# Kernel optimization log

Measured on AMD Instinct MI355X. Metric: run time of the kernel, lower is better.

Reference implementation:

```python
import jax, jax.numpy as jnp
import numpy as np

B, O, GRID = 2048, 48, 112
SIGMA = 5.0


def setup_inputs() -> dict:
    key = jax.random.key(0)
    k1, k2, k3, k4, k5 = jax.random.split(key, 5)
    s = float(GRID - 1)
    xL = jax.random.uniform(k1, (B,), dtype=jnp.float32) * s
    yL = jax.random.uniform(k2, (B,), dtype=jnp.float32) * s
    obj_list = jax.random.uniform(k3, (B, O, 2), dtype=jnp.float32) * s
    obj_num = jax.random.randint(k4, (B,), 0, O + 1, dtype=jnp.int32)
    road_mask = jax.random.randint(k5, (B, GRID, GRID), 0, 2, dtype=jnp.int32)
    return {"xL": xL, "yL": yL, "obj_list": obj_list, "obj_num": obj_num,
            "road_mask": road_mask, "H": GRID, "W": GRID}


def reference(xL, yL, obj_list, obj_num, road_mask, H, W):
    # Faithful vectorization of batch_gaussian_tensor_obj.
    # exp(-(dx^2+dy^2)/(2s^2)) is separable: exp(-dx^2/..) * exp(-dy^2/..),
    # so per-object splats reduce to a batched matmul over the object axis.
    inv = 1.0 / (2.0 * SIGMA * SIGMA)
    x = jnp.arange(H, dtype=jnp.float32)  # row coordinate grid
    y = jnp.arange(W, dtype=jnp.float32)  # col coordinate grid

    # positive goal gaussian, rank-1 outer product per batch element
    gx = jnp.exp(-((x[None, :] - xL[:, None]) ** 2) * inv)  # [B,H]
    gy = jnp.exp(-((y[None, :] - yL[:, None]) ** 2) * inv)  # [B,W]
    goal = gx[:, :, None] * gy[:, None, :]                   # [B,H,W]

    # negative object gaussians; note original swaps xy: xo=xy[1], yo=xy[0]
    xo = obj_list[:, :, 1]  # [B,O] row coords
    yo = obj_list[:, :, 0]  # [B,O] col coords
    ex = jnp.exp(-((x[None, None, :] - xo[:, :, None]) ** 2) * inv)  # [B,O,H]
    ey = jnp.exp(-((y[None, None, :] - yo[:, :, None]) ** 2) * inv)  # [B,O,W]
    valid = (jnp.arange(O)[None, :] < obj_num[:, None]).astype(jnp.float32)  # [B,O]
    obj = jnp.einsum('boh,bow->bhw', ex * valid[:, :, None], ey)     # [B,H,W]

    channel = 0.5 + 0.5 * goal - 0.5 * obj
    channel = jnp.where(road_mask == 0, 0.0, channel)
    return channel
```

## Files before the change

### kernel.cpp

```cpp
#include <hip/hip_runtime.h>

#define GRID_N 112
#define O_MAX 48
#define HW_N (GRID_N * GRID_N)
#define NT 448
#define LSTR 72

typedef _Float16 half8  __attribute__((ext_vector_type(8)));
typedef _Float16 half2v __attribute__((ext_vector_type(2)));
typedef float    f32x4  __attribute__((ext_vector_type(4)));

__global__ __launch_bounds__(NT) void goalmap_kernel(
    const float* __restrict__ xL, const float* __restrict__ yL,
    const float* __restrict__ obj_list, const int* __restrict__ obj_num,
    const int* __restrict__ road_mask, float* __restrict__ out)
{
    constexpr float INV = 1.0f / (2.0f * 5.0f * 5.0f);

    __shared__ _Float16 eyT[GRID_N * LSTR];

    const int b   = blockIdx.x;
    const int tid = threadIdx.x;
    const int n   = obj_num[b];
    const float xl = xL[b];
    const float yl = yL[b];
    const float* ob = obj_list + (size_t)b * O_MAX * 2;

    const int lane = tid & 63;
    const int wid  = tid >> 6;
    const int m    = lane & 15;
    const int quad = lane >> 4;

    const int* rm = road_mask + (size_t)b * HW_N;
    float*     op = out       + (size_t)b * HW_N;

    const int ksteps = (n >= 32) ? 2 : 1;

    float eyy0[8], eyy1[8];
    #pragma unroll
    for (int it = 0; it < 8; ++it) {
        int i  = tid + it * NT;
        int o0 = (i & 31) * 2;
        eyy0[it] = (o0     < n) ? ob[o0 * 2]     : 0.f;
        eyy1[it] = (o0 + 1 < n) ? ob[o0 * 2 + 2] : 0.f;
    }
    float ax0[8], ax1[8];
    #pragma unroll
    for (int j = 0; j < 8; ++j) {
        int k = quad * 8 + j;
        ax0[j] = (k < n)      ? ob[k * 2 + 1]        : 0.f;
        ax1[j] = (k + 32 < n) ? ob[(k + 32) * 2 + 1] : 0.f;
    }

    int mpf[7][4];
    const int base_h = wid * 16 + quad * 4;
    #pragma unroll
    for (int twp = 0; twp < 3; ++twp) {
        int base = base_h * GRID_N + twp * 16 + m;
        #pragma unroll
        for (int r = 0; r < 4; ++r)
            mpf[twp][r] = rm[base + r * GRID_N];
    }

    #pragma unroll
    for (int it = 0; it < 8; ++it) {
        int i   = tid + it * NT;
        int pos = i >> 5;
        int o0  = (i & 31) * 2;
        float fp = (float)pos;
        half2v v;
        {
            float val = 0.f;
            if (o0 <= n) {
                float cy = (o0 < n) ? eyy0[it] : yl;
                float d  = fp - cy;
                val = __expf(-d * d * INV);
            }
            v[0] = (_Float16)val;
        }
        {
            int o = o0 + 1;
            float val = 0.f;
            if (o <= n) {
                float cy = (o < n) ? eyy1[it] : yl;
                float d  = fp - cy;
                val = __expf(-d * d * INV);
            }
            v[1] = (_Float16)val;
        }
        *(half2v*)&eyT[pos * LSTR + o0] = v;
    }

    const float fh = (float)(wid * 16 + m);
    half8 a0, a1;
    #pragma unroll
    for (int j = 0; j < 8; ++j) {
        int k = quad * 8 + j;
        float val = 0.f;
        if (k <= n) {
            float cx = (k < n) ? ax0[j] : xl;
            float s  = (k < n) ? -0.5f  : 0.5f;
            float d  = fh - cx;
            val = s * __expf(-d * d * INV);
        }
        a0[j] = (_Float16)val;
    }
    if (ksteps == 2) {
        #pragma unroll
        for (int j = 0; j < 8; ++j) {
            int k = quad * 8 + j + 32;
            float val = 0.f;
            if (k <= n) {
                float cx = (k < n) ? ax1[j] : xl;
                float s  = (k < n) ? -0.5f  : 0.5f;
                float d  = fh - cx;
                val = s * __expf(-d * d * INV);
            }
            a1[j] = (_Float16)val;
        }
    }

    __builtin_amdgcn_sched_barrier(0);
    asm volatile("s_waitcnt lgkmcnt(0)" ::: "memory");
    __builtin_amdgcn_s_barrier();
    __builtin_amdgcn_sched_barrier(0);

    const int h0 = wid * 16 + quad * 4;
    #pragma unroll
    for (int tw = 0; tw < 7; ++tw) {
        if (tw + 3 < 7) {
            int base = base_h * GRID_N + (tw + 3) * 16 + m;
            #pragma unroll
            for (int r = 0; r < 4; ++r)
                mpf[tw + 3][r] = rm[base + r * GRID_N];
        }
        const _Float16* brow = &eyT[(tw * 16 + m) * LSTR + quad * 8];
        half8 b0 = *(const half8*)brow;
        f32x4 acc = {0.f, 0.f, 0.f, 0.f};
        acc = __builtin_amdgcn_mfma_f32_16x16x32_f16(a0, b0, acc, 0, 0, 0);
        if (ksteps == 2) {
            half8 b1 = *(const half8*)(brow + 32);
            acc = __builtin_amdgcn_mfma_f32_16x16x32_f16(a1, b1, acc, 0, 0, 0);
        }
        int w0 = tw * 16 + m;
        #pragma unroll
        for (int r = 0; r < 4; ++r) {
            float v = 0.5f + acc[r];
            v = (mpf[tw][r] == 0) ? 0.f : v;
            op[(h0 + r) * GRID_N + w0] = v;
        }
    }
}

extern "C" void kernel_launch(void* const* d_in, const int* in_sizes, int n_in,
                              void* d_out, int out_size, void* d_ws, size_t ws_size,
                              hipStream_t stream) {
    const float* xL        = (const float*)d_in[0];
    const float* yL        = (const float*)d_in[1];
    const float* obj_list  = (const float*)d_in[2];
    const int*   obj_num   = (const int*)d_in[3];
    const int*   road_mask = (const int*)d_in[4];
    float*       out       = (float*)d_out;
    const int B = in_sizes[0];

    goalmap_kernel<<<B, NT, 0, stream>>>(xL, yL, obj_list, obj_num, road_mask, out);
}
```

Measured before the change: 210.2 us.

## Process four batch elements per block with double-buffered mask prefetch

Each block now loops over four batch elements instead of one. It double-buffers the shared Gaussian table and prefetches the next element's road mask into registers while computing the current one. The aim is to hide global load latency across elements and spread block launch and setup costs. In exchange the grid shrinks to 512 blocks, which lowers parallelism. Register pressure also rises with 56 mask registers, and the ax0 loads no longer check bounds against n.

```diff
diff --git a/kernel.cpp b/kernel.cpp
--- a/kernel.cpp
+++ b/kernel.cpp
@@ -4,6 +4,7 @@
 #define O_MAX 48
 #define HW_N (GRID_N * GRID_N)
 #define NT 448
+#define NB 4
 #define LSTR 72
 
 typedef _Float16 half8  __attribute__((ext_vector_type(8)));
@@ -13,141 +14,153 @@
 __global__ __launch_bounds__(NT) void goalmap_kernel(
     const float* __restrict__ xL, const float* __restrict__ yL,
     const float* __restrict__ obj_list, const int* __restrict__ obj_num,
-    const int* __restrict__ road_mask, float* __restrict__ out)
+    const int* __restrict__ road_mask, float* __restrict__ out, int B)
 {
     constexpr float INV = 1.0f / (2.0f * 5.0f * 5.0f);
 
-    __shared__ _Float16 eyT[GRID_N * LSTR];
+    __shared__ _Float16 eyT[2][GRID_N * LSTR];
 
-    const int b   = blockIdx.x;
-    const int tid = threadIdx.x;
-    const int n   = obj_num[b];
-    const float xl = xL[b];
-    const float yl = yL[b];
-    const float* ob = obj_list + (size_t)b * O_MAX * 2;
-
+    const int tid  = threadIdx.x;
     const int lane = tid & 63;
     const int wid  = tid >> 6;
     const int m    = lane & 15;
     const int quad = lane >> 4;
+    const int base_h = wid * 16 + quad * 4;
+    const int b0 = blockIdx.x * NB;
 
-    const int* rm = road_mask + (size_t)b * HW_N;
-    float*     op = out       + (size_t)b * HW_N;
+    int mpf[2][7][4];
 
-    const int ksteps = (n >= 32) ? 2 : 1;
+    {
+        const int* rm = road_mask + (size_t)b0 * HW_N;
+        #pragma unroll
+        for (int i = 0; i < 7; ++i) {
+            int base = base_h * GRID_N + i * 16 + m;
+            #pragma unroll
+            for (int r = 0; r < 4; ++r)
+                mpf[0][i][r] = rm[base + r * GRID_N];
+        }
+    }
+    __builtin_amdgcn_sched_barrier(0);
 
-    float eyy0[8], eyy1[8];
-    #pragma unroll
-    for (int it = 0; it < 8; ++it) {
-        int i  = tid + it * NT;
-        int o0 = (i & 31) * 2;
-        eyy0[it] = (o0     < n) ? ob[o0 * 2]     : 0.f;
-        eyy1[it] = (o0 + 1 < n) ? ob[o0 * 2 + 2] : 0.f;
-    }
-    float ax0[8], ax1[8];
-    #pragma unroll
-    for (int j = 0; j < 8; ++j) {
-        int k = quad * 8 + j;
-        ax0[j] = (k < n)      ? ob[k * 2 + 1]        : 0.f;
-        ax1[j] = (k + 32 < n) ? ob[(k + 32) * 2 + 1] : 0.f;
-    }
-
-    int mpf[7][4];
-    const int base_h = wid * 16 + quad * 4;
-    #pragma unroll
-    for (int twp = 0; twp < 3; ++twp) {
-        int base = base_h * GRID_N + twp * 16 + m;
-        #pragma unroll
-        for (int r = 0; r < 4; ++r)
-            mpf[twp][r] = rm[base + r * GRID_N];
-    }
+    const int o0   = (tid & 31) * 2;
+    const int posb = tid >> 5;
+    const float fh = (float)(wid * 16 + m);
 
     #pragma unroll
-    for (int it = 0; it < 8; ++it) {
-        int i   = tid + it * NT;
-        int pos = i >> 5;
-        int o0  = (i & 31) * 2;
-        float fp = (float)pos;
-        half2v v;
-        {
-            float val = 0.f;
-            if (o0 <= n) {
-                float cy = (o0 < n) ? eyy0[it] : yl;
-                float d  = fp - cy;
-                val = __expf(-d * d * INV);
+    for (int j = 0; j < NB; ++j) {
+        const int b = b0 + j;
+        if (b >= B) break;
+        const int cur = j & 1;
+        _Float16* ey = eyT[cur];
+
+        const int n  = obj_num[b];
+        const float xl = xL[b];
+        const float yl = yL[b];
+        const float* ob = obj_list + (size_t)b * (O_MAX * 2);
+
+        float y0 = (o0     < n) ? ob[o0 * 2]     : 0.f;
+        float y1 = (o0 + 1 < n) ? ob[o0 * 2 + 2] : 0.f;
+        float ax0[8], ax1[8];
+        #pragma unroll
+        for (int jj = 0; jj < 8; ++jj) {
+            int k = quad * 8 + jj;
+            ax0[jj] = ob[k * 2 + 1];
+            ax1[jj] = (k + 32 < n) ? ob[k * 2 + 65] : 0.f;
+        }
+        __builtin_amdgcn_sched_barrier(0);
+
+        if (j + 1 < NB && b + 1 < B) {
+            const int* rm = road_mask + (size_t)(b + 1) * HW_N;
+            #pragma unroll
+            for (int i = 0; i < 7; ++i) {
+                int base = base_h * GRID_N + i * 16 + m;
+                #pragma unroll
+                for (int r = 0; r < 4; ++r)
+                    mpf[cur ^ 1][i][r] = rm[base + r * GRID_N];
             }
-            v[0] = (_Float16)val;
         }
-        {
-            int o = o0 + 1;
-            float val = 0.f;
-            if (o <= n) {
-                float cy = (o < n) ? eyy1[it] : yl;
-                float d  = fp - cy;
-                val = __expf(-d * d * INV);
+        __builtin_amdgcn_sched_barrier(0);
+
+        const int ksteps = (n >= 32) ? 2 : 1;
+
+        #pragma unroll
+        for (int it = 0; it < 8; ++it) {
+            int pos  = posb + it * 14;
+            float fp = (float)pos;
+            half2v v;
+            {
+                float val = 0.f;
+                if (o0 <= n) {
+                    float cy = (o0 < n) ? y0 : yl;
+                    float d  = fp - cy;
+                    val = __expf(-d * d * INV);
+                }
+                v[0] = (_Float16)val;
             }
-            v[1] = (_Float16)val;
+            {
+                int o = o0 + 1;
+                float val = 0.f;
+                if (o <= n) {
+                    float cy = (o < n) ? y1 : yl;
+                    float d  = fp - cy;
+                    val = __expf(-d * d * INV);
+                }
+                v[1] = (_Float16)val;
+            }
+            *(half2v*)&ey[pos * LSTR + o0] = v;
         }
-        *(half2v*)&eyT[pos * LSTR + o0] = v;
-    }
 
-    const float fh = (float)(wid * 16 + m);
-    half8 a0, a1;
-    #pragma unroll
-    for (int j = 0; j < 8; ++j) {
-        int k = quad * 8 + j;
-        float val = 0.f;
-        if (k <= n) {
-            float cx = (k < n) ? ax0[j] : xl;
-            float s  = (k < n) ? -0.5f  : 0.5f;
-            float d  = fh - cx;
-            val = s * __expf(-d * d * INV);
-        }
-        a0[j] = (_Float16)val;
-    }
-    if (ksteps == 2) {
+        half8 a0, a1;
         #pragma unroll
-        for (int j = 0; j < 8; ++j) {
-            int k = quad * 8 + j + 32;
+        for (int jj = 0; jj < 8; ++jj) {
+            int k = quad * 8 + jj;
             float val = 0.f;
             if (k <= n) {
-                float cx = (k < n) ? ax1[j] : xl;
+                float cx = (k < n) ? ax0[jj] : xl;
                 float s  = (k < n) ? -0.5f  : 0.5f;
                 float d  = fh - cx;
                 val = s * __expf(-d * d * INV);
             }
-            a1[j] = (_Float16)val;
+            a0[jj] = (_Float16)val;
         }
-    }
+        if (ksteps == 2) {
+            #pragma unroll
+            for (int jj = 0; jj < 8; ++jj) {
+                int k = quad * 8 + jj + 32;
+                float val = 0.f;
+                if (k <= n) {
+                    float cx = (k < n) ? ax1[jj] : xl;
+                    float s  = (k < n) ? -0.5f  : 0.5f;
+                    float d  = fh - cx;
+                    val = s * __expf(-d * d * INV);
+                }
+                a1[jj] = (_Float16)val;
+            }
+        }
 
-    __builtin_amdgcn_sched_barrier(0);
-    asm volatile("s_waitcnt lgkmcnt(0)" ::: "memory");
-    __builtin_amdgcn_s_barrier();
-    __builtin_amdgcn_sched_barrier(0);
+        __builtin_amdgcn_sched_barrier(0);
+        asm volatile("s_waitcnt lgkmcnt(0)" ::: "memory");
+        __builtin_amdgcn_s_barrier();
+        __builtin_amdgcn_sched_barrier(0);
 
-    const int h0 = wid * 16 + quad * 4;
-    #pragma unroll
-    for (int tw = 0; tw < 7; ++tw) {
-        if (tw + 3 < 7) {
-            int base = base_h * GRID_N + (tw + 3) * 16 + m;
+        #pragma unroll
+        for (int tw = 0; tw < 7; ++tw) {
+            const _Float16* brow = &ey[(tw * 16 + m) * LSTR + quad * 8];
+            half8 bf0 = *(const half8*)brow;
+            f32x4 acc = {0.f, 0.f, 0.f, 0.f};
+            acc = __builtin_amdgcn_mfma_f32_16x16x32_f16(a0, bf0, acc, 0, 0, 0);
+            if (ksteps == 2) {
+                half8 bf1 = *(const half8*)(brow + 32);
+                acc = __builtin_amdgcn_mfma_f32_16x16x32_f16(a1, bf1, acc, 0, 0, 0);
+            }
+            float* op = out + (size_t)b * HW_N;
+            int w0 = tw * 16 + m;
             #pragma unroll
-            for (int r = 0; r < 4; ++r)
-                mpf[tw + 3][r] = rm[base + r * GRID_N];
-        }
-        const _Float16* brow = &eyT[(tw * 16 + m) * LSTR + quad * 8];
-        half8 b0 = *(const half8*)brow;
-        f32x4 acc = {0.f, 0.f, 0.f, 0.f};
-        acc = __builtin_amdgcn_mfma_f32_16x16x32_f16(a0, b0, acc, 0, 0, 0);
-        if (ksteps == 2) {
-            half8 b1 = *(const half8*)(brow + 32);
-            acc = __builtin_amdgcn_mfma_f32_16x16x32_f16(a1, b1, acc, 0, 0, 0);
-        }
-        int w0 = tw * 16 + m;
-        #pragma unroll
-        for (int r = 0; r < 4; ++r) {
-            float v = 0.5f + acc[r];
-            v = (mpf[tw][r] == 0) ? 0.f : v;
-            op[(h0 + r) * GRID_N + w0] = v;
+            for (int r = 0; r < 4; ++r) {
+                float v = 0.5f + acc[r];
+                v = (mpf[cur][tw][r] == 0) ? 0.f : v;
+                op[(base_h + r) * GRID_N + w0] = v;
+            }
         }
     }
 }
@@ -163,5 +176,6 @@
     float*       out       = (float*)d_out;
     const int B = in_sizes[0];
 
-    goalmap_kernel<<<B, NT, 0, stream>>>(xL, yL, obj_list, obj_num, road_mask, out);
+    const int grid = (B + NB - 1) / NB;
+    goalmap_kernel<<<grid, NT, 0, stream>>>(xL, yL, obj_list, obj_num, road_mask, out, B);
 }
```

New measurement: 203.2 us. -3.3%, faster.

## Compute B-operand gaussians in registers instead of staging through LDS

Applied to the files above, without the earlier changes.

Removes the shared-memory eyT table, its fill loop and the block-wide barrier. Each wave now computes its own half8 B fragments directly with expf inside the column-tile loop, and all seven road_mask tiles are prefetched up front rather than three ahead. This drops LDS traffic and barrier stalls, but each wave recomputes the column gaussians, so expf work rises about sevenfold. Register pressure also goes up from the full mask prefetch.

```diff
diff --git a/kernel.cpp b/kernel.cpp
--- a/kernel.cpp
+++ b/kernel.cpp
@@ -4,11 +4,9 @@
 #define O_MAX 48
 #define HW_N (GRID_N * GRID_N)
 #define NT 448
-#define LSTR 72
 
-typedef _Float16 half8  __attribute__((ext_vector_type(8)));
-typedef _Float16 half2v __attribute__((ext_vector_type(2)));
-typedef float    f32x4  __attribute__((ext_vector_type(4)));
+typedef _Float16 half8 __attribute__((ext_vector_type(8)));
+typedef float    f32x4 __attribute__((ext_vector_type(4)));
 
 __global__ __launch_bounds__(NT) void goalmap_kernel(
     const float* __restrict__ xL, const float* __restrict__ yL,
@@ -17,79 +15,44 @@
 {
     constexpr float INV = 1.0f / (2.0f * 5.0f * 5.0f);
 
-    __shared__ _Float16 eyT[GRID_N * LSTR];
-
     const int b   = blockIdx.x;
     const int tid = threadIdx.x;
-    const int n   = obj_num[b];
-    const float xl = xL[b];
-    const float yl = yL[b];
-    const float* ob = obj_list + (size_t)b * O_MAX * 2;
-
     const int lane = tid & 63;
     const int wid  = tid >> 6;
     const int m    = lane & 15;
     const int quad = lane >> 4;
 
-    const int* rm = road_mask + (size_t)b * HW_N;
-    float*     op = out       + (size_t)b * HW_N;
+    const int n  = obj_num[b];
+    const float xl = xL[b];
+    const float yl = yL[b];
+    const float* ob = obj_list + (size_t)b * (O_MAX * 2);
+    const int*   rm = road_mask + (size_t)b * HW_N;
+    float*       op = out       + (size_t)b * HW_N;
 
-    const int ksteps = (n >= 32) ? 2 : 1;
-
-    float eyy0[8], eyy1[8];
-    #pragma unroll
-    for (int it = 0; it < 8; ++it) {
-        int i  = tid + it * NT;
-        int o0 = (i & 31) * 2;
-        eyy0[it] = (o0     < n) ? ob[o0 * 2]     : 0.f;
-        eyy1[it] = (o0 + 1 < n) ? ob[o0 * 2 + 2] : 0.f;
-    }
-    float ax0[8], ax1[8];
+    float ax0[8], ay0[8], ax1[8], ay1[8];
     #pragma unroll
     for (int j = 0; j < 8; ++j) {
         int k = quad * 8 + j;
-        ax0[j] = (k < n)      ? ob[k * 2 + 1]        : 0.f;
-        ax1[j] = (k + 32 < n) ? ob[(k + 32) * 2 + 1] : 0.f;
+        ax0[j] = ob[k * 2 + 1];
+        ay0[j] = ob[k * 2];
+        bool g = (k + 32 < n);
+        ax1[j] = g ? ob[(k + 32) * 2 + 1] : 0.f;
+        ay1[j] = g ? ob[(k + 32) * 2]     : 0.f;
     }
+    __builtin_amdgcn_sched_barrier(0);
 
     int mpf[7][4];
-    const int base_h = wid * 16 + quad * 4;
+    const int h0 = wid * 16 + quad * 4;
     #pragma unroll
-    for (int twp = 0; twp < 3; ++twp) {
-        int base = base_h * GRID_N + twp * 16 + m;
+    for (int i = 0; i < 7; ++i) {
+        int base = h0 * GRID_N + i * 16 + m;
         #pragma unroll
         for (int r = 0; r < 4; ++r)
-            mpf[twp][r] = rm[base + r * GRID_N];
+            mpf[i][r] = rm[base + r * GRID_N];
     }
+    __builtin_amdgcn_sched_barrier(0);
 
-    #pragma unroll
-    for (int it = 0; it < 8; ++it) {
-        int i   = tid + it * NT;
-        int pos = i >> 5;
-        int o0  = (i & 31) * 2;
-        float fp = (float)pos;
-        half2v v;
-        {
-            float val = 0.f;
-            if (o0 <= n) {
-                float cy = (o0 < n) ? eyy0[it] : yl;
-                float d  = fp - cy;
-                val = __expf(-d * d * INV);
-            }
-            v[0] = (_Float16)val;
-        }
-        {
-            int o = o0 + 1;
-            float val = 0.f;
-            if (o <= n) {
-                float cy = (o < n) ? eyy1[it] : yl;
-                float d  = fp - cy;
-                val = __expf(-d * d * INV);
-            }
-            v[1] = (_Float16)val;
-        }
-        *(half2v*)&eyT[pos * LSTR + o0] = v;
-    }
+    const int ksteps = (n >= 32) ? 2 : 1;
 
     const float fh = (float)(wid * 16 + m);
     half8 a0, a1;
@@ -120,29 +83,40 @@
         }
     }
 
-    __builtin_amdgcn_sched_barrier(0);
-    asm volatile("s_waitcnt lgkmcnt(0)" ::: "memory");
-    __builtin_amdgcn_s_barrier();
-    __builtin_amdgcn_sched_barrier(0);
-
-    const int h0 = wid * 16 + quad * 4;
     #pragma unroll
     for (int tw = 0; tw < 7; ++tw) {
-        if (tw + 3 < 7) {
-            int base = base_h * GRID_N + (tw + 3) * 16 + m;
-            #pragma unroll
-            for (int r = 0; r < 4; ++r)
-                mpf[tw + 3][r] = rm[base + r * GRID_N];
+        const float fw = (float)(tw * 16 + m);
+        half8 b0;
+        #pragma unroll
+        for (int j = 0; j < 8; ++j) {
+            int k = quad * 8 + j;
+            float val = 0.f;
+            if (k <= n) {
+                float cy = (k < n) ? ay0[j] : yl;
+                float d  = fw - cy;
+                val = __expf(-d * d * INV);
+            }
+            b0[j] = (_Float16)val;
         }
-        const _Float16* brow = &eyT[(tw * 16 + m) * LSTR + quad * 8];
-        half8 b0 = *(const half8*)brow;
         f32x4 acc = {0.f, 0.f, 0.f, 0.f};
         acc = __builtin_amdgcn_mfma_f32_16x16x32_f16(a0, b0, acc, 0, 0, 0);
         if (ksteps == 2) {
-            half8 b1 = *(const half8*)(brow + 32);
+            half8 b1;
+            #pragma unroll
+            for (int j = 0; j < 8; ++j) {
+                int k = quad * 8 + j + 32;
+                float val = 0.f;
+                if (k <= n) {
+                    float cy = (k < n) ? ay1[j] : yl;
+                    float d  = fw - cy;
+                    val = __expf(-d * d * INV);
+                }
+                b1[j] = (_Float16)val;
+            }
             acc = __builtin_amdgcn_mfma_f32_16x16x32_f16(a1, b1, acc, 0, 0, 0);
         }
-        int w0 = tw * 16 + m;
+
+        const int w0 = tw * 16 + m;
         #pragma unroll
         for (int r = 0; r < 4; ++r) {
             float v = 0.5f + acc[r];
```

New measurement: 208.4 us. No clear change (-0.8%).
